# Kernel optimization log

Measured on AMD Instinct MI355X. Metric: run time of the kernel, lower is better.

## Reference

```python
import jax, jax.numpy as jnp
import numpy as np

NU = 500000   # num user nodes
NI = 100000   # num item nodes
F  = 300      # item feature dim
D  = 64       # hidden channels
E  = 2000000  # num rated edges
EL = 1000000  # num supervision (label) edges


def setup_inputs() -> dict:
    key = jax.random.key(0)
    ks = jax.random.split(key, 24)
    def nrm(k, shp, scale=0.05):
        return jax.random.normal(k, shp, dtype=jnp.float32) * scale
    inp = {
        "user_emb_w": nrm(ks[0], (NU, D)),
        "item_x": jax.random.normal(ks[1], (NI, F), dtype=jnp.float32),
        "item_lin_w": nrm(ks[2], (F, D)),
        "item_lin_b": jnp.zeros((D,), jnp.float32),
        "Wl1_ui": nrm(ks[3], (D, D)), "Wr1_ui": nrm(ks[4], (D, D)), "b1_ui": jnp.zeros((D,), jnp.float32),
        "Wl1_iu": nrm(ks[5], (D, D)), "Wr1_iu": nrm(ks[6], (D, D)), "b1_iu": jnp.zeros((D,), jnp.float32),
        "Wl2_ui": nrm(ks[7], (D, D)), "Wr2_ui": nrm(ks[8], (D, D)), "b2_ui": jnp.zeros((D,), jnp.float32),
        "Wl2_iu": nrm(ks[9], (D, D)), "Wr2_iu": nrm(ks[10], (D, D)), "b2_iu": jnp.zeros((D,), jnp.float32),
        "user_node_id": jnp.arange(NU, dtype=jnp.int32),
        "edge_src": jax.random.randint(ks[11], (E,), 0, NU, dtype=jnp.int32),
        "edge_dst": jax.random.randint(ks[12], (E,), 0, NI, dtype=jnp.int32),
        "label_src": jax.random.randint(ks[13], (EL,), 0, NU, dtype=jnp.int32),
        "label_dst": jax.random.randint(ks[14], (EL,), 0, NI, dtype=jnp.int32),
    }
    return inp


def _seg_mean(x_src, src, dst, n_dst):
    # mean-aggregate source features onto destination nodes (PyG SAGEConv aggr='mean')
    s = jax.ops.segment_sum(x_src[src], dst, num_segments=n_dst)
    c = jax.ops.segment_sum(jnp.ones(src.shape, x_src.dtype), dst, num_segments=n_dst)
    return s / jnp.maximum(c, 1.0)[:, None]


def reference(user_emb_w, item_x, item_lin_w, item_lin_b,
              Wl1_ui, Wr1_ui, b1_ui, Wl1_iu, Wr1_iu, b1_iu,
              Wl2_ui, Wr2_ui, b2_ui, Wl2_iu, Wr2_iu, b2_iu,
              user_node_id, edge_src, edge_dst, label_src, label_dst):
    # input layers: user embedding lookup, item linear projection
    x_user = user_emb_w[user_node_id]                 # [NU, D]
    x_item = item_x @ item_lin_w + item_lin_b         # [NI, D]

    def hetero_sage(xu, xi, Wl_ui, Wr_ui, bui, Wl_iu, Wr_iu, biu):
        # edge type (user, rates, item): aggregate user msgs at items
        hi = _seg_mean(xu, edge_src, edge_dst, NI) @ Wl_ui + bui + xi @ Wr_ui
        # edge type (item, rev_rates, user): aggregate item msgs at users
        hu = _seg_mean(xi, edge_dst, edge_src, NU) @ Wl_iu + biu + xu @ Wr_iu
        return hu, hi

    hu, hi = hetero_sage(x_user, x_item, Wl1_ui, Wr1_ui, b1_ui, Wl1_iu, Wr1_iu, b1_iu)
    hu, hi = jax.nn.relu(hu), jax.nn.relu(hi)
    hu, hi = hetero_sage(hu, hi, Wl2_ui, Wr2_ui, b2_ui, Wl2_iu, Wr2_iu, b2_iu)

    # DOT predictor on edge_label_index pairs
    return jnp.sum(hu[label_src] * hi[label_dst], axis=-1)   # [EL]
```

## Files before the change

### kernel.cpp

```cpp
#include <hip/hip_runtime.h>

#define NUu 500000
#define NIi 100000
#define FDIM 300
#define DDIM 64
#define NEe 2000000
#define ELl 1000000

#define BSZL_I 8
#define BSZL_U 9
#define NB_I 391
#define NB_U 977
#define NBT (NB_I + NB_U)
#define SH_I 19
#define SH_U 17

typedef __attribute__((ext_vector_type(8))) short s8v;
typedef __attribute__((ext_vector_type(4))) short s4v;
typedef __attribute__((ext_vector_type(4))) float f4v;
typedef unsigned short u16;

__device__ __forceinline__ float bf2f(u16 h) {
    union { unsigned u; float f; } x; x.u = ((unsigned)h) << 16; return x.f;
}
__device__ __forceinline__ u16 f2bf(float f) {
    union { float f; unsigned u; } x; x.f = f;
    unsigned u = x.u;
    u += 0x7FFFu + ((u >> 16) & 1u);
    return (u16)(u >> 16);
}

__global__ __launch_bounds__(256) void k_cast_users(const float* __restrict__ ue,
                                                    const int* __restrict__ uid,
                                                    u16* __restrict__ xu) {
    int idx = blockIdx.x * 256 + threadIdx.x;
    int n  = idx >> 4;
    int d0 = (idx & 15) * 4;
    int src = uid[n];
    const float4* p = (const float4*)(ue + (size_t)src * DDIM + d0);
    float4 v = *p;
    s4v o;
    o[0] = (short)f2bf(v.x); o[1] = (short)f2bf(v.y);
    o[2] = (short)f2bf(v.z); o[3] = (short)f2bf(v.w);
    *(s4v*)(xu + (size_t)n * DDIM + d0) = o;
}

__global__ __launch_bounds__(256) void k_cast_w(const float* __restrict__ W,
                                                u16* __restrict__ wbf) {
    int idx = blockIdx.x * 256 + threadIdx.x;
    if (idx >= 2560) return;
    int f = idx >> 6, lane = idx & 63;
    int q = lane >> 4, c = lane & 15;
    int kstep = f >> 2, nb = f & 3;
    u16* dst = wbf + (size_t)idx * 8;
#pragma unroll
    for (int j = 0; j < 8; j++) {
        int k = kstep * 32 + q * 8 + j;
        float v = (k < FDIM) ? W[k * DDIM + nb * 16 + c] : 0.f;
        dst[j] = f2bf(v);
    }
}

__global__ __launch_bounds__(256) void k_item_lin2(const float* __restrict__ ix,
                                                   const u16* __restrict__ wbf,
                                                   const float* __restrict__ b,
                                                   u16* __restrict__ xi) {
    __shared__ __align__(16) u16 wl[40 * 64 * 8];
    int tid = threadIdx.x;
    for (int i = tid; i < 2560; i += 256)
        ((f4v*)wl)[i] = ((const f4v*)wbf)[i];
    __syncthreads();

    int lane = tid & 63;
    int q = lane >> 4, c = lane & 15;
    float bv[4];
#pragma unroll
    for (int nb = 0; nb < 4; nb++) bv[nb] = b[nb * 16 + c];

    int w = blockIdx.x * 4 + (tid >> 6);
    int stride = gridDim.x * 4;
    const int NT = NIi / 16;
    for (int t = w; t < NT; t += stride) {
        int row = t * 16 + c;
        const float* xr = ix + (size_t)row * FDIM;
        f4v acc[4];
#pragma unroll
        for (int nb = 0; nb < 4; nb++) {
            acc[nb][0] = bv[nb]; acc[nb][1] = bv[nb];
            acc[nb][2] = bv[nb]; acc[nb][3] = bv[nb];
        }
#pragma unroll
        for (int ks = 0; ks < 10; ks++) {
            s8v a;
            if (ks < 9 || q == 0) {
                float4 v0 = *(const float4*)(xr + ks * 32 + q * 8);
                float4 v1 = *(const float4*)(xr + ks * 32 + q * 8 + 4);
                a[0] = (short)f2bf(v0.x); a[1] = (short)f2bf(v0.y);
                a[2] = (short)f2bf(v0.z); a[3] = (short)f2bf(v0.w);
                a[4] = (short)f2bf(v1.x); a[5] = (short)f2bf(v1.y);
                a[6] = (short)f2bf(v1.z); a[7] = (short)f2bf(v1.w);
            } else {
                float4 v0 = *(const float4*)(xr + 296);
                a[0] = (short)f2bf(v0.x); a[1] = (short)f2bf(v0.y);
                a[2] = (short)f2bf(v0.z); a[3] = (short)f2bf(v0.w);
                a[4] = 0; a[5] = 0; a[6] = 0; a[7] = 0;
            }
#pragma unroll
            for (int nb = 0; nb < 4; nb++) {
                s8v bb = *(const s8v*)(wl + ((size_t)(ks * 4 + nb) * 64 + lane) * 8);
                acc[nb] = __builtin_amdgcn_mfma_f32_16x16x32_bf16(a, bb, acc[nb], 0, 0, 0);
            }
        }
#pragma unroll
        for (int nb = 0; nb < 4; nb++)
#pragma unroll
            for (int r = 0; r < 4; r++)
                xi[(size_t)(t * 16 + q * 4 + r) * DDIM + nb * 16 + c] = f2bf(acc[nb][r]);
    }
}

__global__ __launch_bounds__(256) void k_hist(const int* __restrict__ src,
                                              const int* __restrict__ dst,
                                              int* __restrict__ hist) {
    __shared__ int h[NBT];
    int t = threadIdx.x;
    for (int c = t; c < NBT; c += 256) h[c] = 0;
    __syncthreads();
    int base = blockIdx.x * 2048;
#pragma unroll
    for (int k = 0; k < 8; k++) {
        int e = base + k * 256 + t;
        if (e < NEe) {
            int s = src[e], d = dst[e];
            atomicAdd(&h[d >> BSZL_I], 1);
            atomicAdd(&h[NB_I + (s >> BSZL_U)], 1);
        }
    }
    __syncthreads();
    for (int c = t; c < NBT; c += 256) {
        int n = h[c];
        if (n) atomicAdd(&hist[c], n);
    }
}

__device__ __forceinline__ void scanN(const int* __restrict__ cnt, int n, int total,
                                      int* __restrict__ base, int* __restrict__ frontier,
                                      int* sb) {
    int t = threadIdx.x;
    int v[8]; int s = 0;
#pragma unroll
    for (int i = 0; i < 8; i++) {
        int idx = t * 8 + i;
        v[i] = (idx < n) ? cnt[idx] : 0;
        s += v[i];
    }
    sb[t] = s; __syncthreads();
    for (int o = 1; o < 256; o <<= 1) {
        int a = (t >= o) ? sb[t - o] : 0;
        __syncthreads();
        sb[t] += a;
        __syncthreads();
    }
    int run = sb[t] - s;
#pragma unroll
    for (int i = 0; i < 8; i++) {
        int idx = t * 8 + i;
        if (idx < n) { base[idx] = run; frontier[idx] = run; }
        run += v[i];
    }
    if (t == 0) base[n] = total;
    __syncthreads();
}

__global__ __launch_bounds__(256) void k_bucket_scan(const int* __restrict__ hist,
                                                     int* __restrict__ base_i, int* __restrict__ fr_i,
                                                     int* __restrict__ base_u, int* __restrict__ fr_u,
                                                     int* __restrict__ rpi, int* __restrict__ rpu) {
    __shared__ int sb[256];
    scanN(hist, NB_I, NEe, base_i, fr_i, sb);
    scanN(hist + NB_I, NB_U, NEe, base_u, fr_u, sb);
    if (threadIdx.x == 0) { rpi[NIi] = NEe; rpu[NUu] = NEe; }
}

__global__ __launch_bounds__(256) void k_scatter(const int* __restrict__ src,
                                                 const int* __restrict__ dst,
                                                 int* __restrict__ fr_i, int* __restrict__ fr_u,
                                                 unsigned* __restrict__ scat_i,
                                                 unsigned* __restrict__ scat_u) {
    __shared__ int h[NBT];
    int t = threadIdx.x;
    for (int c = t; c < NBT; c += 256) h[c] = 0;
    __syncthreads();
    int base = blockIdx.x * 2048;
#pragma unroll
    for (int k = 0; k < 8; k++) {
        int e = base + k * 256 + t;
        if (e < NEe) {
            int s = src[e], d = dst[e];
            atomicAdd(&h[d >> BSZL_I], 1);
            atomicAdd(&h[NB_I + (s >> BSZL_U)], 1);
        }
    }
    __syncthreads();
    for (int c = t; c < NBT; c += 256) {
        int n = h[c];
        if (n) {
            int b = (c < NB_I) ? atomicAdd(&fr_i[c], n) : atomicAdd(&fr_u[c - NB_I], n);
            h[c] = b;
        }
    }
    __syncthreads();
#pragma unroll
    for (int k = 0; k < 8; k++) {
        int e = base + k * 256 + t;
        if (e < NEe) {
            int s = src[e], d = dst[e];
            int p = atomicAdd(&h[d >> BSZL_I], 1);
            scat_i[p] = (unsigned)s | ((unsigned)(d & 255) << SH_I);
            int q = atomicAdd(&h[NB_I + (s >> BSZL_U)], 1);
            scat_u[q] = (unsigned)d | ((unsigned)(s & 511) << SH_U);
        }
    }
}

__global__ __launch_bounds__(256) void k_bfill(const unsigned* __restrict__ scat,
                                               const int* __restrict__ base,
                                               int* __restrict__ rp, int* __restrict__ col,
                                               int shift, int bszlog, int ntotal) {
    __shared__ int cnt[512];
    __shared__ int pos[512];
    __shared__ int sb[256];
    int b = blockIdx.x;
    int t = threadIdx.x;
    int e0 = base[b], e1 = base[b + 1];
    int node0 = b << bszlog;
    int bsz = 1 << bszlog;
    unsigned mask = (1u << shift) - 1u;

    for (int c = t; c < bsz; c += 256) cnt[c] = 0;
    __syncthreads();
    for (int e = e0 + t; e < e1; e += 256) {
        unsigned v = scat[e];
        atomicAdd(&cnt[v >> shift], 1);
    }
    __syncthreads();
    int per = bsz >> 8;
    int loc[2]; int ls = 0;
#pragma unroll
    for (int i = 0; i < 2; i++) {
        loc[i] = (i < per) ? cnt[t * per + i] : 0;
        ls += loc[i];
    }
    sb[t] = ls; __syncthreads();
    for (int o = 1; o < 256; o <<= 1) {
        int a = (t >= o) ? sb[t - o] : 0;
        __syncthreads();
        sb[t] += a;
        __syncthreads();
    }
    int run = e0 + sb[t] - ls;
#pragma unroll
    for (int i = 0; i < 2; i++) {
        if (i < per) {
            int idx = t * per + i;
            int node = node0 + idx;
            if (node < ntotal) rp[node] = run;
            pos[idx] = run;
            run += loc[i];
        }
    }
    __syncthreads();
    for (int e = e0 + t; e < e1; e += 256) {
        unsigned v = scat[e];
        int l = v >> shift;
        int p = atomicAdd(&pos[l], 1);
        col[p] = (int)(v & mask);
    }
}

__global__ __launch_bounds__(256) void k_agg(const u16* __restrict__ feat,
                                             u16* __restrict__ out,
                                             const int* __restrict__ rp,
                                             const int* __restrict__ col, int n) {
    int lane = threadIdx.x & 63;
    int g = lane >> 4;
    int t = lane & 15;
    int w = blockIdx.x * 4 + (threadIdx.x >> 6);
    int stride = gridDim.x * 4;
    for (int node = w; node < n; node += stride) {
        int s0 = rp[node], s1 = rp[node + 1];
        float a0 = 0.f, a1 = 0.f, a2 = 0.f, a3 = 0.f;
        int j = s0 + g;
        for (; j + 4 < s1; j += 8) {
            int r0 = col[j], r1 = col[j + 4];
            s4v v0 = *(const s4v*)(feat + (size_t)r0 * DDIM + t * 4);
            s4v v1 = *(const s4v*)(feat + (size_t)r1 * DDIM + t * 4);
            a0 += bf2f((u16)v0[0]) + bf2f((u16)v1[0]);
            a1 += bf2f((u16)v0[1]) + bf2f((u16)v1[1]);
            a2 += bf2f((u16)v0[2]) + bf2f((u16)v1[2]);
            a3 += bf2f((u16)v0[3]) + bf2f((u16)v1[3]);
        }
        if (j < s1) {
            int r = col[j];
            s4v v = *(const s4v*)(feat + (size_t)r * DDIM + t * 4);
            a0 += bf2f((u16)v[0]); a1 += bf2f((u16)v[1]);
            a2 += bf2f((u16)v[2]); a3 += bf2f((u16)v[3]);
        }
        a0 += __shfl_xor(a0, 16); a0 += __shfl_xor(a0, 32);
        a1 += __shfl_xor(a1, 16); a1 += __shfl_xor(a1, 32);
        a2 += __shfl_xor(a2, 16); a2 += __shfl_xor(a2, 32);
        a3 += __shfl_xor(a3, 16); a3 += __shfl_xor(a3, 32);
        if (g == 0) {
            int deg = s1 - s0;
            float sc = deg > 0 ? 1.0f / (float)deg : 0.f;
            s4v o;
            o[0] = (short)f2bf(a0 * sc); o[1] = (short)f2bf(a1 * sc);
            o[2] = (short)f2bf(a2 * sc); o[3] = (short)f2bf(a3 * sc);
            *(s4v*)(out + (size_t)node * DDIM + t * 4) = o;
        }
    }
}

__global__ __launch_bounds__(256) void k_transform(const u16* __restrict__ aggf,
                                                   const u16* __restrict__ xf,
                                                   const float* __restrict__ Wl,
                                                   const float* __restrict__ Wr,
                                                   const float* __restrict__ bias,
                                                   u16* __restrict__ out,
                                                   int ntiles, int relu) {
    int lane = threadIdx.x & 63;
    int q = lane >> 4, c = lane & 15;
    int w = blockIdx.x * 4 + (threadIdx.x >> 6);
    int stride = gridDim.x * 4;

    s8v wl[2][4], wrg[2][4];
#pragma unroll
    for (int ks = 0; ks < 2; ks++)
#pragma unroll
        for (int nb = 0; nb < 4; nb++) {
            s8v fl, fr;
#pragma unroll
            for (int j = 0; j < 8; j++) {
                int row = ks * 32 + q * 8 + j;
                int cc = nb * 16 + c;
                fl[j] = (short)f2bf(Wl[row * DDIM + cc]);
                fr[j] = (short)f2bf(Wr[row * DDIM + cc]);
            }
            wl[ks][nb] = fl; wrg[ks][nb] = fr;
        }
    float bv[4];
#pragma unroll
    for (int nb = 0; nb < 4; nb++) bv[nb] = bias[nb * 16 + c];

    for (int t = w; t < ntiles; t += stride) {
        const s8v* pa = (const s8v*)(aggf + (size_t)(t * 16 + c) * DDIM + q * 8);
        const s8v* px = (const s8v*)(xf   + (size_t)(t * 16 + c) * DDIM + q * 8);
        s8v a0 = pa[0], a1 = pa[4], x0 = px[0], x1 = px[4];
        f4v acc[4];
#pragma unroll
        for (int nb = 0; nb < 4; nb++) {
            acc[nb][0] = bv[nb]; acc[nb][1] = bv[nb];
            acc[nb][2] = bv[nb]; acc[nb][3] = bv[nb];
        }
#pragma unroll
        for (int nb = 0; nb < 4; nb++) {
            acc[nb] = __builtin_amdgcn_mfma_f32_16x16x32_bf16(a0, wl[0][nb],  acc[nb], 0, 0, 0);
            acc[nb] = __builtin_amdgcn_mfma_f32_16x16x32_bf16(a1, wl[1][nb],  acc[nb], 0, 0, 0);
            acc[nb] = __builtin_amdgcn_mfma_f32_16x16x32_bf16(x0, wrg[0][nb], acc[nb], 0, 0, 0);
            acc[nb] = __builtin_amdgcn_mfma_f32_16x16x32_bf16(x1, wrg[1][nb], acc[nb], 0, 0, 0);
        }
#pragma unroll
        for (int nb = 0; nb < 4; nb++)
#pragma unroll
            for (int r = 0; r < 4; r++) {
                float v = acc[nb][r];
                if (relu) v = fmaxf(v, 0.f);
                out[(size_t)(t * 16 + q * 4 + r) * DDIM + nb * 16 + c] = f2bf(v);
            }
    }
}

__global__ __launch_bounds__(256) void k_dot(const u16* __restrict__ hu,
                                             const u16* __restrict__ hi,
                                             const int* __restrict__ ls,
                                             const int* __restrict__ ld,
                                             float* __restrict__ out) {
    int lane = threadIdx.x & 63;
    int sub = lane >> 3, t8 = lane & 7;
    int w = blockIdx.x * 4 + (threadIdx.x >> 6);
    int stride = gridDim.x * 4;
    const int ngroups = ELl / 8;
    for (int g = w; g < ngroups; g += stride) {
        int e = g * 8 + sub;
        int u = ls[e], it = ld[e];
        s8v av = *(const s8v*)(hu + (size_t)u  * DDIM + t8 * 8);
        s8v bv = *(const s8v*)(hi + (size_t)it * DDIM + t8 * 8);
        float s = 0.f;
#pragma unroll
        for (int k = 0; k < 8; k++) s += bf2f((u16)av[k]) * bf2f((u16)bv[k]);
        s += __shfl_xor(s, 4);
        s += __shfl_xor(s, 2);
        s += __shfl_xor(s, 1);
        if (t8 == 0) out[e] = s;
    }
}

extern "C" void kernel_launch(void* const* d_in, const int* in_sizes, int n_in,
                              void* d_out, int out_size, void* d_ws, size_t ws_size,
                              hipStream_t stream) {
    const float* user_emb = (const float*)d_in[0];
    const float* item_x   = (const float*)d_in[1];
    const float* item_w   = (const float*)d_in[2];
    const float* item_b   = (const float*)d_in[3];
    const float* Wl1_ui = (const float*)d_in[4];
    const float* Wr1_ui = (const float*)d_in[5];
    const float* b1_ui  = (const float*)d_in[6];
    const float* Wl1_iu = (const float*)d_in[7];
    const float* Wr1_iu = (const float*)d_in[8];
    const float* b1_iu  = (const float*)d_in[9];
    const float* Wl2_ui = (const float*)d_in[10];
    const float* Wr2_ui = (const float*)d_in[11];
    const float* b2_ui  = (const float*)d_in[12];
    const float* Wl2_iu = (const float*)d_in[13];
    const float* Wr2_iu = (const float*)d_in[14];
    const float* b2_iu  = (const float*)d_in[15];
    const int* uid  = (const int*)d_in[16];
    const int* esrc = (const int*)d_in[17];
    const int* edst = (const int*)d_in[18];
    const int* lsrc = (const int*)d_in[19];
    const int* ldst = (const int*)d_in[20];
    float* out = (float*)d_out;

    char* ws = (char*)d_ws;
    size_t off = 0;
    auto alloc = [&](size_t bytes) -> void* {
        void* p = ws + off;
        off += (bytes + 255) & ~(size_t)255;
        return p;
    };
    u16* xu_b   = (u16*)alloc((size_t)NUu * DDIM * 2);
    u16* hu1_b  = (u16*)alloc((size_t)NUu * DDIM * 2);
    u16* aggu_b = (u16*)alloc((size_t)NUu * DDIM * 2);
    u16* xi_b   = (u16*)alloc((size_t)NIi * DDIM * 2);
    u16* hi1_b  = (u16*)alloc((size_t)NIi * DDIM * 2);
    u16* aggi_b = (u16*)alloc((size_t)NIi * DDIM * 2);
    int* coli = (int*)alloc((size_t)NEe * 4);
    int* colu = (int*)alloc((size_t)NEe * 4);
    int* rpi  = (int*)alloc((size_t)(NIi + 1) * 4);
    int* rpu  = (int*)alloc((size_t)(NUu + 1) * 4);
    int* hist   = (int*)alloc((size_t)NBT * 4);
    int* base_i = (int*)alloc((size_t)(NB_I + 1) * 4);
    int* base_u = (int*)alloc((size_t)(NB_U + 1) * 4);
    int* fr_i   = (int*)alloc((size_t)NB_I * 4);
    int* fr_u   = (int*)alloc((size_t)NB_U * 4);
    u16* wbf    = (u16*)alloc((size_t)40 * 64 * 8 * 2);
    unsigned* scat_i = (unsigned*)xu_b;
    unsigned* scat_u = (unsigned*)((char*)xu_b + (size_t)NEe * 4);

    hipMemsetAsync(hist, 0, (size_t)NBT * 4, stream);
    int nchunks = (NEe + 2047) / 2048;
    k_hist<<<nchunks, 256, 0, stream>>>(esrc, edst, hist);
    k_bucket_scan<<<1, 256, 0, stream>>>(hist, base_i, fr_i, base_u, fr_u, rpi, rpu);
    k_scatter<<<nchunks, 256, 0, stream>>>(esrc, edst, fr_i, fr_u, scat_i, scat_u);
    k_bfill<<<NB_I, 256, 0, stream>>>(scat_i, base_i, rpi, coli, SH_I, BSZL_I, NIi);
    k_bfill<<<NB_U, 256, 0, stream>>>(scat_u, base_u, rpu, colu, SH_U, BSZL_U, NUu);

    k_cast_w<<<10, 256, 0, stream>>>(item_w, wbf);
    k_cast_users<<<NUu * 16 / 256, 256, 0, stream>>>(user_emb, uid, xu_b);
    k_item_lin2<<<512, 256, 0, stream>>>(item_x, wbf, item_b, xi_b);

    const int NT_I = NIi / 16;
    const int NT_U = NUu / 16;

    k_agg<<<2048, 256, 0, stream>>>(xu_b, aggi_b, rpi, coli, NIi);
    k_transform<<<512, 256, 0, stream>>>(aggi_b, xi_b, Wl1_ui, Wr1_ui, b1_ui, hi1_b, NT_I, 1);
    k_agg<<<2048, 256, 0, stream>>>(xi_b, aggu_b, rpu, colu, NUu);
    k_transform<<<1024, 256, 0, stream>>>(aggu_b, xu_b, Wl1_iu, Wr1_iu, b1_iu, hu1_b, NT_U, 1);

    k_agg<<<2048, 256, 0, stream>>>(hu1_b, aggi_b, rpi, coli, NIi);
    k_transform<<<512, 256, 0, stream>>>(aggi_b, hi1_b, Wl2_ui, Wr2_ui, b2_ui, aggi_b, NT_I, 0);
    k_agg<<<2048, 256, 0, stream>>>(hi1_b, aggu_b, rpu, colu, NUu);
    k_transform<<<1024, 256, 0, stream>>>(aggu_b, hu1_b, Wl2_iu, Wr2_iu, b2_iu, aggu_b, NT_U, 0);

    k_dot<<<2048, 256, 0, stream>>>(aggu_b, aggi_b, lsrc, ldst, out);
}
```

Measured before the change: 906.9 us.

## Fuse mean aggregation with SAGE transform into one MFMA kernel per layer

Replaces the separate k_agg and k_transform passes with a single k_fused kernel. In it, each lane of a 16-node tile gathers the neighbour rows of its own node, builds the mean-aggregated bf16 MFMA fragment in registers, and multiplies it against the weights held in shared memory. The weights are pre-cast to bf16 fragments once by a new k_cast_w8 kernel. This removes the write and re-read of the aggregated buffer and four kernel launches. The cost is that each lane now walks its own node's edge list, so a wave runs as long as the highest-degree node in its tile, and the gathers are less coalesced than the old per-node wave layout.

```diff
diff --git a/kernel.cpp b/kernel.cpp
--- a/kernel.cpp
+++ b/kernel.cpp
@@ -6,6 +6,7 @@
 #define DDIM 64
 #define NEe 2000000
 #define ELl 1000000
+#define EMAX (NEe - 1)
 
 #define BSZL_I 8
 #define BSZL_U 9
@@ -58,6 +59,33 @@
         int k = kstep * 32 + q * 8 + j;
         float v = (k < FDIM) ? W[k * DDIM + nb * 16 + c] : 0.f;
         dst[j] = f2bf(v);
+    }
+}
+
+__global__ __launch_bounds__(256) void k_cast_w8(
+    const float* __restrict__ W0, const float* __restrict__ W1,
+    const float* __restrict__ W2, const float* __restrict__ W3,
+    const float* __restrict__ W4, const float* __restrict__ W5,
+    const float* __restrict__ W6, const float* __restrict__ W7,
+    u16* __restrict__ out) {
+    int idx = blockIdx.x * 256 + threadIdx.x;
+    if (idx >= 4096) return;
+    int wm = idx >> 9;
+    int s = idx & 511;
+    int ks = s >> 8, nb = (s >> 6) & 3, lane = s & 63;
+    int q = lane >> 4, c = lane & 15;
+    const float* W;
+    switch (wm) {
+        case 0: W = W0; break; case 1: W = W1; break;
+        case 2: W = W2; break; case 3: W = W3; break;
+        case 4: W = W4; break; case 5: W = W5; break;
+        case 6: W = W6; break; default: W = W7; break;
+    }
+    u16* dst = out + (size_t)idx * 8;
+#pragma unroll
+    for (int j = 0; j < 8; j++) {
+        int row = ks * 32 + q * 8 + j;
+        dst[j] = f2bf(W[row * DDIM + nb * 16 + c]);
     }
 }
 
@@ -278,96 +306,90 @@
     }
 }
 
-__global__ __launch_bounds__(256) void k_agg(const u16* __restrict__ feat,
-                                             u16* __restrict__ out,
-                                             const int* __restrict__ rp,
-                                             const int* __restrict__ col, int n) {
-    int lane = threadIdx.x & 63;
-    int g = lane >> 4;
-    int t = lane & 15;
-    int w = blockIdx.x * 4 + (threadIdx.x >> 6);
+__global__ __launch_bounds__(256) void k_fused(const u16* __restrict__ feat,
+                                               const u16* __restrict__ xf,
+                                               const u16* __restrict__ wfrag,
+                                               const float* __restrict__ bias,
+                                               u16* __restrict__ out,
+                                               const int* __restrict__ rp,
+                                               const int* __restrict__ col,
+                                               int ntiles, int relu) {
+    __shared__ __align__(16) u16 wsh[8192];
+    int tid = threadIdx.x;
+    for (int i = tid; i < 1024; i += 256)
+        ((f4v*)wsh)[i] = ((const f4v*)wfrag)[i];
+    __syncthreads();
+
+    int lane = tid & 63;
+    int q = lane >> 4, c = lane & 15;
+    int w = blockIdx.x * 4 + (tid >> 6);
     int stride = gridDim.x * 4;
-    for (int node = w; node < n; node += stride) {
+    float bv[4];
+#pragma unroll
+    for (int nb = 0; nb < 4; nb++) bv[nb] = bias[nb * 16 + c];
+
+    for (int t = w; t < ntiles; t += stride) {
+        int node = t * 16 + c;
         int s0 = rp[node], s1 = rp[node + 1];
-        float a0 = 0.f, a1 = 0.f, a2 = 0.f, a3 = 0.f;
-        int j = s0 + g;
-        for (; j + 4 < s1; j += 8) {
-            int r0 = col[j], r1 = col[j + 4];
-            s4v v0 = *(const s4v*)(feat + (size_t)r0 * DDIM + t * 4);
-            s4v v1 = *(const s4v*)(feat + (size_t)r1 * DDIM + t * 4);
-            a0 += bf2f((u16)v0[0]) + bf2f((u16)v1[0]);
-            a1 += bf2f((u16)v0[1]) + bf2f((u16)v1[1]);
-            a2 += bf2f((u16)v0[2]) + bf2f((u16)v1[2]);
-            a3 += bf2f((u16)v0[3]) + bf2f((u16)v1[3]);
-        }
-        if (j < s1) {
-            int r = col[j];
-            s4v v = *(const s4v*)(feat + (size_t)r * DDIM + t * 4);
-            a0 += bf2f((u16)v[0]); a1 += bf2f((u16)v[1]);
-            a2 += bf2f((u16)v[2]); a3 += bf2f((u16)v[3]);
-        }
-        a0 += __shfl_xor(a0, 16); a0 += __shfl_xor(a0, 32);
-        a1 += __shfl_xor(a1, 16); a1 += __shfl_xor(a1, 32);
-        a2 += __shfl_xor(a2, 16); a2 += __shfl_xor(a2, 32);
-        a3 += __shfl_xor(a3, 16); a3 += __shfl_xor(a3, 32);
-        if (g == 0) {
-            int deg = s1 - s0;
-            float sc = deg > 0 ? 1.0f / (float)deg : 0.f;
-            s4v o;
-            o[0] = (short)f2bf(a0 * sc); o[1] = (short)f2bf(a1 * sc);
-            o[2] = (short)f2bf(a2 * sc); o[3] = (short)f2bf(a3 * sc);
-            *(s4v*)(out + (size_t)node * DDIM + t * 4) = o;
-        }
-    }
-}
-
-__global__ __launch_bounds__(256) void k_transform(const u16* __restrict__ aggf,
-                                                   const u16* __restrict__ xf,
-                                                   const float* __restrict__ Wl,
-                                                   const float* __restrict__ Wr,
-                                                   const float* __restrict__ bias,
-                                                   u16* __restrict__ out,
-                                                   int ntiles, int relu) {
-    int lane = threadIdx.x & 63;
-    int q = lane >> 4, c = lane & 15;
-    int w = blockIdx.x * 4 + (threadIdx.x >> 6);
-    int stride = gridDim.x * 4;
-
-    s8v wl[2][4], wrg[2][4];
-#pragma unroll
-    for (int ks = 0; ks < 2; ks++)
-#pragma unroll
-        for (int nb = 0; nb < 4; nb++) {
-            s8v fl, fr;
+        int deg = s1 - s0;
+        float inv = (deg > 0) ? 1.0f / (float)deg : 0.0f;
+
+        const s8v* px = (const s8v*)(xf + (size_t)node * DDIM + q * 8);
+        s8v x0 = px[0], x1 = px[4];
+
+        float accA[8] = {0.f, 0.f, 0.f, 0.f, 0.f, 0.f, 0.f, 0.f};
+        float accB[8] = {0.f, 0.f, 0.f, 0.f, 0.f, 0.f, 0.f, 0.f};
+
+        for (int i = 0; __any(i < deg); i += 2) {
+            int ia = s0 + i;
+            int ea = min(ia, EMAX);
+            int eb = min(ia + 1, EMAX);
+            int ra = col[ea];
+            int rb = col[eb];
+            float ma = (i < deg) ? inv : 0.f;
+            float mb = (i + 1 < deg) ? inv : 0.f;
+            const u16* fa = feat + (size_t)ra * DDIM + q * 8;
+            const u16* fb = feat + (size_t)rb * DDIM + q * 8;
+            s8v va0 = *(const s8v*)fa;
+            s8v va1 = *(const s8v*)(fa + 32);
+            s8v vb0 = *(const s8v*)fb;
+            s8v vb1 = *(const s8v*)(fb + 32);
 #pragma unroll
             for (int j = 0; j < 8; j++) {
-                int row = ks * 32 + q * 8 + j;
-                int cc = nb * 16 + c;
-                fl[j] = (short)f2bf(Wl[row * DDIM + cc]);
-                fr[j] = (short)f2bf(Wr[row * DDIM + cc]);
+                accA[j] = fmaf(ma, bf2f((u16)va0[j]), accA[j]);
+                accB[j] = fmaf(ma, bf2f((u16)va1[j]), accB[j]);
+                accA[j] = fmaf(mb, bf2f((u16)vb0[j]), accA[j]);
+                accB[j] = fmaf(mb, bf2f((u16)vb1[j]), accB[j]);
             }
-            wl[ks][nb] = fl; wrg[ks][nb] = fr;
-        }
-    float bv[4];
-#pragma unroll
-    for (int nb = 0; nb < 4; nb++) bv[nb] = bias[nb * 16 + c];
-
-    for (int t = w; t < ntiles; t += stride) {
-        const s8v* pa = (const s8v*)(aggf + (size_t)(t * 16 + c) * DDIM + q * 8);
-        const s8v* px = (const s8v*)(xf   + (size_t)(t * 16 + c) * DDIM + q * 8);
-        s8v a0 = pa[0], a1 = pa[4], x0 = px[0], x1 = px[4];
+        }
+
+        s8v a0, a1;
+#pragma unroll
+        for (int j = 0; j < 8; j++) {
+            a0[j] = (short)f2bf(accA[j]);
+            a1[j] = (short)f2bf(accB[j]);
+        }
+
         f4v acc[4];
 #pragma unroll
         for (int nb = 0; nb < 4; nb++) {
             acc[nb][0] = bv[nb]; acc[nb][1] = bv[nb];
             acc[nb][2] = bv[nb]; acc[nb][3] = bv[nb];
         }
+
+        unsigned lz = (unsigned)lane * 8u;
+        asm volatile("" : "+v"(lz));
+        const u16* wb = wsh + lz;
 #pragma unroll
         for (int nb = 0; nb < 4; nb++) {
-            acc[nb] = __builtin_amdgcn_mfma_f32_16x16x32_bf16(a0, wl[0][nb],  acc[nb], 0, 0, 0);
-            acc[nb] = __builtin_amdgcn_mfma_f32_16x16x32_bf16(a1, wl[1][nb],  acc[nb], 0, 0, 0);
-            acc[nb] = __builtin_amdgcn_mfma_f32_16x16x32_bf16(x0, wrg[0][nb], acc[nb], 0, 0, 0);
-            acc[nb] = __builtin_amdgcn_mfma_f32_16x16x32_bf16(x1, wrg[1][nb], acc[nb], 0, 0, 0);
+            s8v wl0 = *(const s8v*)(wb + nb * 512);
+            s8v wl1 = *(const s8v*)(wb + 2048 + nb * 512);
+            s8v wr0 = *(const s8v*)(wb + 4096 + nb * 512);
+            s8v wr1 = *(const s8v*)(wb + 6144 + nb * 512);
+            acc[nb] = __builtin_amdgcn_mfma_f32_16x16x32_bf16(a0, wl0, acc[nb], 0, 0, 0);
+            acc[nb] = __builtin_amdgcn_mfma_f32_16x16x32_bf16(a1, wl1, acc[nb], 0, 0, 0);
+            acc[nb] = __builtin_amdgcn_mfma_f32_16x16x32_bf16(x0, wr0, acc[nb], 0, 0, 0);
+            acc[nb] = __builtin_amdgcn_mfma_f32_16x16x32_bf16(x1, wr1, acc[nb], 0, 0, 0);
         }
 #pragma unroll
         for (int nb = 0; nb < 4; nb++)
@@ -440,10 +462,10 @@
     };
     u16* xu_b   = (u16*)alloc((size_t)NUu * DDIM * 2);
     u16* hu1_b  = (u16*)alloc((size_t)NUu * DDIM * 2);
-    u16* aggu_b = (u16*)alloc((size_t)NUu * DDIM * 2);
+    u16* hu2_b  = (u16*)alloc((size_t)NUu * DDIM * 2);
     u16* xi_b   = (u16*)alloc((size_t)NIi * DDIM * 2);
     u16* hi1_b  = (u16*)alloc((size_t)NIi * DDIM * 2);
-    u16* aggi_b = (u16*)alloc((size_t)NIi * DDIM * 2);
+    u16* hi2_b  = (u16*)alloc((size_t)NIi * DDIM * 2);
     int* coli = (int*)alloc((size_t)NEe * 4);
     int* colu = (int*)alloc((size_t)NEe * 4);
     int* rpi  = (int*)alloc((size_t)(NIi + 1) * 4);
@@ -454,6 +476,7 @@
     int* fr_i   = (int*)alloc((size_t)NB_I * 4);
     int* fr_u   = (int*)alloc((size_t)NB_U * 4);
     u16* wbf    = (u16*)alloc((size_t)40 * 64 * 8 * 2);
+    u16* wfrag2 = (u16*)alloc((size_t)4 * 8192 * 2);
     unsigned* scat_i = (unsigned*)xu_b;
     unsigned* scat_u = (unsigned*)((char*)xu_b + (size_t)NEe * 4);
 
@@ -466,21 +489,22 @@
     k_bfill<<<NB_U, 256, 0, stream>>>(scat_u, base_u, rpu, colu, SH_U, BSZL_U, NUu);
 
     k_cast_w<<<10, 256, 0, stream>>>(item_w, wbf);
+    k_cast_w8<<<16, 256, 0, stream>>>(Wl1_ui, Wr1_ui, Wl1_iu, Wr1_iu,
+                                      Wl2_ui, Wr2_ui, Wl2_iu, Wr2_iu, wfrag2);
     k_cast_users<<<NUu * 16 / 256, 256, 0, stream>>>(user_emb, uid, xu_b);
     k_item_lin2<<<512, 256, 0, stream>>>(item_x, wbf, item_b, xi_b);
 
     const int NT_I = NIi / 16;
     const int NT_U = NUu / 16;
 
-    k_agg<<<2048, 256, 0, stream>>>(xu_b, aggi_b, rpi, coli, NIi);
-    k_transform<<<512, 256, 0, stream>>>(aggi_b, xi_b, Wl1_ui, Wr1_ui, b1_ui, hi1_b, NT_I, 1);
-    k_agg<<<2048, 256, 0, stream>>>(xi_b, aggu_b, rpu, colu, NUu);
-    k_transform<<<1024, 256, 0, stream>>>(aggu_b, xu_b, Wl1_iu, Wr1_iu, b1_iu, hu1_b, NT_U, 1);
-
-    k_agg<<<2048, 256, 0, stream>>>(hu1_b, aggi_b, rpi, coli, NIi);
-    k_transform<<<512, 256, 0, stream>>>(aggi_b, hi1_b, Wl2_ui, Wr2_ui, b2_ui, aggi_b, NT_I, 0);
-    k_agg<<<2048, 256, 0, stream>>>(hi1_b, aggu_b, rpu, colu, NUu);
-    k_transform<<<1024, 256, 0, stream>>>(aggu_b, hu1_b, Wl2_iu, Wr2_iu, b2_iu, aggu_b, NT_U, 0);
-
-    k_dot<<<2048, 256, 0, stream>>>(aggu_b, aggi_b, lsrc, ldst, out);
-}
+    k_fused<<<512, 256, 0, stream>>>(xu_b, xi_b, wfrag2 + 0 * 8192, b1_ui,
+                                     hi1_b, rpi, coli, NT_I, 1);
+    k_fused<<<2048, 256, 0, stream>>>(xi_b, xu_b, wfrag2 + 1 * 8192, b1_iu,
+                                      hu1_b, rpu, colu, NT_U, 1);
+    k_fused<<<512, 256, 0, stream>>>(hu1_b, hi1_b, wfrag2 + 2 * 8192, b2_ui,
+                                     hi2_b, rpi, coli, NT_I, 0);
+    k_fused<<<2048, 256, 0, stream>>>(hi1_b, hu1_b, wfrag2 + 3 * 8192, b2_iu,
+                                      hu2_b, rpu, colu, NT_U, 0);
+
+    k_dot<<<2048, 256, 0, stream>>>(hu2_b, hi2_b, lsrc, ldst, out);
+}
```

New measurement: 850.8 us. -6.2%, faster.
